# Optimization experiments

Measured on AMD Instinct MI355X. Metric: run time of the kernel, lower is better.

Reference implementation:

```python
import jax, jax.numpy as jnp
import numpy as np

WORD_VOCAB, WORD_DIM = 50257, 512
CHAR_VOCAB, CHAR_DIM = 262, 128
OUT_DIM = 1024
B, SW, SC = 32, 256, 16
EMB_DIM = WORD_DIM + CHAR_DIM


def setup_inputs() -> dict:
    key = jax.random.key(0)
    ks = jax.random.split(key, 12)
    word_inputs = jax.random.randint(ks[0], (B, SW), 0, WORD_VOCAB)
    char_ids = jax.random.randint(ks[1], (B, SW, SC), 0, CHAR_VOCAB)
    char_lengths = jax.random.randint(ks[2], (B, SW), 1, SC + 1)  # at least 1 char
    word_table = jax.random.normal(ks[3], (WORD_VOCAB, WORD_DIM), jnp.float32) * 0.02
    char_table = jax.random.normal(ks[4], (CHAR_VOCAB, CHAR_DIM), jnp.float32) * 0.02
    # RecursiveCell: gate = Linear(2d -> 3d), project = Linear(2d -> d)
    Wg = jax.random.normal(ks[5], (3 * CHAR_DIM, 2 * CHAR_DIM), jnp.float32) * (1.0 / np.sqrt(2 * CHAR_DIM))
    bg = jnp.zeros((3 * CHAR_DIM,), jnp.float32)
    Wp = jax.random.normal(ks[6], (CHAR_DIM, 2 * CHAR_DIM), jnp.float32) * (1.0 / np.sqrt(2 * CHAR_DIM))
    bp = jnp.zeros((CHAR_DIM,), jnp.float32)
    # final projection Linear(emb_dim -> output_dim)
    W_out = jax.random.normal(ks[7], (OUT_DIM, EMB_DIM), jnp.float32) * (1.0 / np.sqrt(EMB_DIM))
    b_out = jnp.zeros((OUT_DIM,), jnp.float32)
    return {"word_inputs": word_inputs, "char_ids": char_ids, "char_lengths": char_lengths,
            "word_table": word_table, "char_table": char_table,
            "Wg": Wg, "bg": bg, "Wp": Wp, "bp": bp, "W_out": W_out, "b_out": b_out}


def reference(word_inputs, char_ids, char_lengths, word_table, char_table, Wg, bg, Wp, bp, W_out, b_out):
    b, sw = word_inputs.shape
    sc = char_ids.shape[-1]
    d = char_table.shape[-1]
    n = b * sw

    word_emb = word_table[word_inputs]                      # [B, SW, WORD_DIM]

    ids = char_ids.reshape(n, sc)
    lens = char_lengths.reshape(n, 1)
    layer0 = char_table[ids]                                # [N, SC, d]
    pos = jnp.arange(sc)

    def step(layer, length):
        # vectorized RecursiveCell over all adjacent pairs i in [0, SC-2]
        left = layer[:, :-1, :]                             # [N, SC-1, d]
        right = layer[:, 1:, :]                             # [N, SC-1, d]
        flat = jnp.concatenate([left, right], axis=-1)      # [N, SC-1, 2d]
        z = flat @ Wp.T + bp                                # [N, SC-1, d]
        g = jax.nn.softmax((flat @ Wg.T + bg).reshape(n, sc - 1, 3, d), axis=2)
        ret = g[:, :, 0] * left + g[:, :, 1] * right + g[:, :, 2] * z
        new_layer = jnp.pad(ret, ((0, 0), (0, 1), (0, 0)))  # positions >= SC-1 stay zero
        # masked_scatter_: update position i iff i < len - length
        mask = (pos[None, :] < (lens - length))[..., None]  # [N, SC, 1]
        return jnp.where(mask, new_layer, layer), None

    layer, _ = jax.lax.scan(step, layer0, jnp.arange(1, sc))
    char_repr = layer[:, 0, :].reshape(b, sw, d)            # [B, SW, d]

    token_embedding = jnp.concatenate([word_emb, char_repr], axis=-1)
    return token_embedding @ W_out.T + b_out                # [B, SW, OUT_DIM]
```

## Files before the change

### kernel.cpp

```cpp
#include <hip/hip_runtime.h>
#include <hip/hip_bf16.h>

#define NTOK 8192
#define SCC  16
#define CD   128
#define WD   512
#define OD   1024
#define ED   640
#define TW   4
#define SP   132
#define ST   (SCC * SP)

typedef __attribute__((ext_vector_type(8))) short short8;
typedef __attribute__((ext_vector_type(4))) float f32x4;

__device__ __forceinline__ unsigned short f2bf(float f) {
    union { float f; unsigned u; } v; v.f = f;
    unsigned r = v.u + 0x7FFF + ((v.u >> 16) & 1);
    return (unsigned short)(r >> 16);
}

__global__ void sort_zero(int* s) { if (threadIdx.x < 48) s[threadIdx.x] = 0; }

__global__ void sort_hist(const int* __restrict__ lengths, int* __restrict__ s) {
    const int i = blockIdx.x * 256 + threadIdx.x;
    if (i < NTOK) atomicAdd(&s[lengths[i] - 1], 1);
}

__global__ void sort_prefix(int* s) {
    if (threadIdx.x == 0) {
        int acc = 0;
        for (int b = 15; b >= 0; --b) { s[16 + b] = acc; acc += s[b]; }
    }
}

__global__ __launch_bounds__(256) void sort_scatter_det(
    const int* __restrict__ lengths, int* __restrict__ s)
{
    __shared__ int wsum[4];
    __shared__ int running;
    const int b   = blockIdx.x;
    const int tid = threadIdx.x;
    if (tid == 0) running = s[16 + b];
    __syncthreads();
    for (int c0 = 0; c0 < NTOK; c0 += 256) {
        const int i = c0 + tid;
        const bool f = (lengths[i] - 1 == b);
        const unsigned long long m = __ballot(f);
        const int wv = tid >> 6;
        if ((tid & 63) == 0) wsum[wv] = __popcll(m);
        __syncthreads();
        int excl = 0;
#pragma unroll
        for (int k = 0; k < 4; ++k) if (k < wv) excl += wsum[k];
        const int lanerank = __popcll(m & ((1ull << (tid & 63)) - 1ull));
        if (f) s[48 + running + excl + lanerank] = i;
        const int tot = wsum[0] + wsum[1] + wsum[2] + wsum[3];
        __syncthreads();
        if (tid == 0) running += tot;
        __syncthreads();
    }
}

__global__ __launch_bounds__(256) void pack_weights(
    const float* __restrict__ Wg, const float* __restrict__ Wp,
    uint4* __restrict__ packed)
{
    const int gid  = blockIdx.x * 256 + threadIdx.x;
    const int lane = gid & 63;
    const int kf   = (gid >> 6) & 7;
    const int c    = (gid >> 9) & 3;
    const int w    = (gid >> 11) & 7;
    const int n    = c * 128 + w * 16 + (lane & 15);
    const int k0   = kf * 32 + (lane >> 4) * 8;
    const float* src = (n < 384) ? (Wg + n * 256 + k0) : (Wp + (n - 384) * 256 + k0);
    uint4 o;
    o.x = f2bf(src[0]) | ((unsigned)f2bf(src[1]) << 16);
    o.y = f2bf(src[2]) | ((unsigned)f2bf(src[3]) << 16);
    o.z = f2bf(src[4]) | ((unsigned)f2bf(src[5]) << 16);
    o.w = f2bf(src[6]) | ((unsigned)f2bf(src[7]) << 16);
    packed[gid] = o;
}

__global__ __launch_bounds__(256) void pack_wout(
    const float* __restrict__ W_out, uint4* __restrict__ packed)
{
    const int gid  = blockIdx.x * 256 + threadIdx.x;
    const int lane = gid & 63;
    const int kf   = (gid >> 6) % 20;
    const int nb   = (gid >> 6) / 20;
    const int n    = nb * 16 + (lane & 15);
    const int k0   = kf * 32 + (lane >> 4) * 8;
    const float* src = W_out + (size_t)n * ED + k0;
    uint4 o;
    o.x = f2bf(src[0]) | ((unsigned)f2bf(src[1]) << 16);
    o.y = f2bf(src[2]) | ((unsigned)f2bf(src[3]) << 16);
    o.z = f2bf(src[4]) | ((unsigned)f2bf(src[5]) << 16);
    o.w = f2bf(src[6]) | ((unsigned)f2bf(src[7]) << 16);
    packed[gid] = o;
}

#define LOAD_B(DST, KF)                                                     \
    {                                                                       \
        const uint4* wp_ = Wpacked + (w * 32 + (KF)) * 64 + lane;           \
        union { uint4 u; short8 s; } cv0, cv1, cv2, cv3;                    \
        cv0.u = wp_[0];    DST[0] = cv0.s;                                  \
        cv1.u = wp_[512];  DST[1] = cv1.s;                                  \
        cv2.u = wp_[1024]; DST[2] = cv2.s;                                  \
        cv3.u = wp_[1536]; DST[3] = cv3.s;                                  \
    }

#define LOAD_B_LDS(DST, KFI)                                                \
    {                                                                       \
        const uint4* sp_ = SW + ((w * 3 + (KFI)) * 4) * 64 + lane;          \
        union { uint4 u; short8 s; } d0, d1, d2, d3;                        \
        d0.u = sp_[0];   DST[0] = d0.s;                                     \
        d1.u = sp_[64];  DST[1] = d1.s;                                     \
        d2.u = sp_[128]; DST[2] = d2.s;                                     \
        d3.u = sp_[192]; DST[3] = d3.s;                                     \
    }

#define MFMA_PHASE(BV, KF)                                                  \
    {                                                                       \
        _Pragma("unroll")                                                   \
        for (int m_ = 0; m_ < 4; ++m_) {                                    \
            if (m_ < mfrags) {                                              \
                const int r_ = m_ * 16 + col + (((KF) >= 4) ? 4 : 0);       \
                int ba_ = (r_ << 8) + (((KF) & 3) << 6) + (q << 4);         \
                ba_ ^= (r_ & 15) << 4;                                      \
                const short8 a_ = *reinterpret_cast<const short8*>(         \
                    reinterpret_cast<const char*>(X) + ba_);                \
                acc[m_][0] = __builtin_amdgcn_mfma_f32_16x16x32_bf16(a_, BV[0], acc[m_][0], 0, 0, 0); \
                acc[m_][1] = __builtin_amdgcn_mfma_f32_16x16x32_bf16(a_, BV[1], acc[m_][1], 0, 0, 0); \
                acc[m_][2] = __builtin_amdgcn_mfma_f32_16x16x32_bf16(a_, BV[2], acc[m_][2], 0, 0, 0); \
                acc[m_][3] = __builtin_amdgcn_mfma_f32_16x16x32_bf16(a_, BV[3], acc[m_][3], 0, 0, 0); \
            }                                                               \
        }                                                                   \
    }

__global__ __launch_bounds__(512, 2) void scan_mfma(
    const int*   __restrict__ char_ids,
    const int*   __restrict__ char_lengths,
    const float* __restrict__ char_table,
    const float* __restrict__ bg, const float* __restrict__ bp,
    const uint4* __restrict__ Wpacked,
    const int*   __restrict__ order,
    unsigned short* __restrict__ char_repr)
{
    __shared__ __align__(16) float S[TW * ST];
    __shared__ __align__(16) unsigned short X[68 * 128];
    __shared__ __align__(16) uint4 SW[8 * 3 * 4 * 64];
    __shared__ int toksh[TW];
    __shared__ int Lsh[TW];

    const int tid  = threadIdx.x;
    const int lane = tid & 63;
    const int w    = tid >> 6;
    const int col  = lane & 15;
    const int q    = lane >> 4;

    if (tid < TW) {
        const int tok = order[blockIdx.x * TW + tid];
        toksh[tid] = tok;
        Lsh[tid]   = char_lengths[tok];
    }

    const int dj = w * 16 + col;
    const float b02 = bg[dj] - bg[256 + dj];
    const float b12 = bg[128 + dj] - bg[256 + dj];
    const float bz  = bp[dj];

    short8 bpin0[4], bpin1[4];
    LOAD_B(bpin0, 0);
    LOAD_B(bpin1, 1);

#pragma unroll
    for (int kfi = 0; kfi < 3; ++kfi)
#pragma unroll
        for (int c = 0; c < 4; ++c)
            SW[((w * 3 + kfi) * 4 + c) * 64 + lane] =
                Wpacked[(w * 32 + c * 8 + (2 + kfi)) * 64 + lane];

    __syncthreads();

    for (int i = tid; i < TW * SCC * (CD / 4); i += 512) {
        const int t   = i >> 9;
        const int rem = i & 511;
        const int c   = rem >> 5;
        const int d4  = rem & 31;
        const int id  = char_ids[toksh[t] * SCC + c];
        const float4 v = reinterpret_cast<const float4*>(char_table + id * CD)[d4];
        *reinterpret_cast<float4*>(S + t * ST + c * SP + d4 * 4) = v;
    }

    int L[TW];
#pragma unroll
    for (int t = 0; t < TW; ++t) L[t] = Lsh[t];
    const int maxL = max(max(L[0], L[1]), max(L[2], L[3]));

    __syncthreads();

    for (int i = tid; i < 68 * 64; i += 512) {
        const int r  = i >> 6;
        const int ku = i & 63;
        unsigned u = 0u;
        if (r < 60) {
            const int p = r >> 2, t = r & 3;
            const float2 v = *reinterpret_cast<const float2*>(S + t * ST + p * SP + 2 * ku);
            u = f2bf(v.x) | ((unsigned)f2bf(v.y) << 16);
        }
        int ba = (r << 8) + (ku << 2);
        ba ^= (r & 15) << 4;
        *reinterpret_cast<unsigned*>(reinterpret_cast<char*>(X) + ba) = u;
    }
    __syncthreads();

    for (int len = 1; len < maxL; ++len) {
        const int Amax   = maxL - len;
        const int mfrags = (4 * Amax + 15) >> 4;

        f32x4 acc[4][4];
#pragma unroll
        for (int m = 0; m < 4; ++m)
#pragma unroll
            for (int c = 0; c < 4; ++c) acc[m][c] = (f32x4){0.f, 0.f, 0.f, 0.f};

        short8 bA[4], bB[4], bL[4];
        LOAD_B(bA, 5);
        LOAD_B(bB, 6);
        MFMA_PHASE(bpin0, 0);
        LOAD_B_LDS(bL, 0);
        MFMA_PHASE(bpin1, 1);
        MFMA_PHASE(bL, 2);
        LOAD_B_LDS(bL, 1);
        MFMA_PHASE(bL, 3);
        LOAD_B_LDS(bL, 2);
        MFMA_PHASE(bL, 4);
        MFMA_PHASE(bA, 5);
        LOAD_B(bA, 7);
        MFMA_PHASE(bB, 6);
        MFMA_PHASE(bA, 7);

#pragma unroll
        for (int m = 0; m < 4; ++m) {
            if (m < mfrags) {
                const int p = m * 4 + q;
#pragma unroll
                for (int i = 0; i < 4; ++i) {
                    const float a0  = acc[m][0][i];
                    const float a1  = acc[m][1][i];
                    const float a2v = acc[m][2][i];
                    const float z   = acc[m][3][i] + bz;
                    const float E0  = __expf(a0 - a2v + b02);
                    const float E1  = __expf(a1 - a2v + b12);
                    const float left  = S[i * ST + p * SP + dj];
                    const float right = S[i * ST + (p + 1) * SP + dj];
                    const float inv = __builtin_amdgcn_rcpf(E0 + E1 + 1.0f);
                    acc[m][0][i] = (E0 * left + E1 * right + z) * inv;
                }
            }
        }
        __syncthreads();

#pragma unroll
        for (int m = 0; m < 4; ++m) {
            if (m < mfrags) {
                const int p = m * 4 + q;
#pragma unroll
                for (int i = 0; i < 4; ++i) {
                    const float val = acc[m][0][i];
                    if (p < L[i] - len) S[i * ST + p * SP + dj] = val;
                    const unsigned short bv = f2bf(val);
                    const int rl = m * 16 + q * 4 + i;
                    int bl = (rl << 8) + (dj << 1);
                    bl ^= (rl & 15) << 4;
                    *reinterpret_cast<unsigned short*>(
                        reinterpret_cast<char*>(X) + bl) = bv;
                }
            }
        }
        __syncthreads();
    }

    for (int i = tid; i < TW * CD; i += 512) {
        const int t = i >> 7, d = i & 127;
        char_repr[toksh[t] * CD + d] = f2bf(S[t * ST + d]);
    }
}

__global__ __launch_bounds__(256) void out_mfma(
    const int*   __restrict__ word_inputs,
    const float* __restrict__ word_table,
    const unsigned short* __restrict__ char_repr,
    const uint4* __restrict__ pwout,
    const float* __restrict__ b_out,
    float*       __restrict__ out)
{
    __shared__ __align__(16) unsigned short E[16 * ED];

    const int tg   = blockIdx.x * 16;
    const int tid  = threadIdx.x;
    const int lane = tid & 63;
    const int w    = tid >> 6;
    const int col  = lane & 15;
    const int q    = lane >> 4;

    for (int i = tid; i < 16 * 256; i += 256) {
        const int rt = i >> 8, kp = i & 255;
        const float2 v = *reinterpret_cast<const float2*>(
            word_table + (size_t)word_inputs[tg + rt] * WD + 2 * kp);
        const unsigned u = f2bf(v.x) | ((unsigned)f2bf(v.y) << 16);
        int baddr = rt * 1280 + kp * 4;
        baddr ^= (rt & 7) << 4;
        *reinterpret_cast<unsigned*>(reinterpret_cast<char*>(E) + baddr) = u;
    }
    for (int i = tid; i < 16 * 64; i += 256) {
        const int rt = i >> 6, kp = i & 63;
        const unsigned u = *reinterpret_cast<const unsigned*>(
            char_repr + (tg + rt) * CD + 2 * kp);
        int baddr = rt * 1280 + 1024 + kp * 4;
        baddr ^= (rt & 7) << 4;
        *reinterpret_cast<unsigned*>(reinterpret_cast<char*>(E) + baddr) = u;
    }
    __syncthreads();

    f32x4 acc[16];
#pragma unroll
    for (int nf = 0; nf < 16; ++nf) acc[nf] = (f32x4){0.f, 0.f, 0.f, 0.f};

#pragma unroll 4
    for (int kf = 0; kf < 20; ++kf) {
        int ba = col * 1280 + kf * 64 + q * 16;
        ba ^= (col & 7) << 4;
        const short8 a = *reinterpret_cast<const short8*>(
            reinterpret_cast<const char*>(E) + ba);
#pragma unroll
        for (int nf = 0; nf < 16; ++nf) {
            const int nb = w * 16 + nf;
            union { uint4 u; short8 s; } cv;
            cv.u = pwout[(nb * 20 + kf) * 64 + lane];
            acc[nf] = __builtin_amdgcn_mfma_f32_16x16x32_bf16(a, cv.s, acc[nf], 0, 0, 0);
        }
    }

#pragma unroll
    for (int nf = 0; nf < 16; ++nf) {
        const int j = (w * 16 + nf) * 16 + col;
        const float bias = b_out[j];
#pragma unroll
        for (int i = 0; i < 4; ++i) {
            out[(size_t)(tg + q * 4 + i) * OD + j] = acc[nf][i] + bias;
        }
    }
}


extern "C" void kernel_launch(void* const* d_in, const int* in_sizes, int n_in,
                              void* d_out, int out_size, void* d_ws, size_t ws_size,
                              hipStream_t stream)
{
    const int*   word_inputs  = (const int*)  d_in[0];
    const int*   char_ids     = (const int*)  d_in[1];
    const int*   char_lengths = (const int*)  d_in[2];
    const float* word_table   = (const float*)d_in[3];
    const float* char_table   = (const float*)d_in[4];
    const float* Wg           = (const float*)d_in[5];
    const float* bg           = (const float*)d_in[6];
    const float* Wp           = (const float*)d_in[7];
    const float* bp           = (const float*)d_in[8];
    const float* W_out        = (const float*)d_in[9];
    const float* b_out        = (const float*)d_in[10];

    float* out = (float*)d_out;
    char* ws = (char*)d_ws;
    unsigned short* char_repr = (unsigned short*)ws;
    uint4* Wpacked = (uint4*)(ws + 2 * 1024 * 1024);
    int*   sortbuf = (int*)(ws + 2 * 1024 * 1024 + 256 * 1024);
    const int* order = sortbuf + 48;
    uint4* pwout = (uint4*)(ws + 2 * 1024 * 1024 + 256 * 1024 + 64 * 1024);

    pack_weights<<<64, 256, 0, stream>>>(Wg, Wp, Wpacked);
    pack_wout<<<320, 256, 0, stream>>>(W_out, pwout);
    sort_zero<<<1, 64, 0, stream>>>(sortbuf);
    sort_hist<<<NTOK / 256, 256, 0, stream>>>(char_lengths, sortbuf);
    sort_prefix<<<1, 64, 0, stream>>>(sortbuf);
    sort_scatter_det<<<16, 256, 0, stream>>>(char_lengths, sortbuf);

    scan_mfma<<<NTOK / TW, 512, 0, stream>>>(char_ids, char_lengths, char_table,
                                             bg, bp, Wpacked, order, char_repr);
    out_mfma<<<NTOK / 16, 256, 0, stream>>>(word_inputs, word_table, char_repr,
                                            pwout, b_out, out);
}
```

Before: 270.9 us.

## Keep scan state in registers with shuffles; retile output GEMM to 32 tokens

```diff
diff --git a/kernel.cpp b/kernel.cpp
--- a/kernel.cpp
+++ b/kernel.cpp
@@ -8,8 +8,6 @@
 #define OD   1024
 #define ED   640
 #define TW   4
-#define SP   132
-#define ST   (SCC * SP)
 
 typedef __attribute__((ext_vector_type(8))) short short8;
 typedef __attribute__((ext_vector_type(4))) float f32x4;
@@ -147,7 +145,6 @@
     const int*   __restrict__ order,
     unsigned short* __restrict__ char_repr)
 {
-    __shared__ __align__(16) float S[TW * ST];
     __shared__ __align__(16) unsigned short X[68 * 128];
     __shared__ __align__(16) uint4 SW[8 * 3 * 4 * 64];
     __shared__ int toksh[TW];
@@ -183,35 +180,37 @@
 
     __syncthreads();
 
-    for (int i = tid; i < TW * SCC * (CD / 4); i += 512) {
-        const int t   = i >> 9;
-        const int rem = i & 511;
-        const int c   = rem >> 5;
-        const int d4  = rem & 31;
-        const int id  = char_ids[toksh[t] * SCC + c];
-        const float4 v = reinterpret_cast<const float4*>(char_table + id * CD)[d4];
-        *reinterpret_cast<float4*>(S + t * ST + c * SP + d4 * 4) = v;
-    }
-
     int L[TW];
 #pragma unroll
-    for (int t = 0; t < TW; ++t) L[t] = Lsh[t];
+    for (int i = 0; i < TW; ++i) L[i] = Lsh[i];
     const int maxL = max(max(L[0], L[1]), max(L[2], L[3]));
 
-    __syncthreads();
-
-    for (int i = tid; i < 68 * 64; i += 512) {
-        const int r  = i >> 6;
-        const int ku = i & 63;
-        unsigned u = 0u;
-        if (r < 60) {
-            const int p = r >> 2, t = r & 3;
-            const float2 v = *reinterpret_cast<const float2*>(S + t * ST + p * SP + 2 * ku);
-            u = f2bf(v.x) | ((unsigned)f2bf(v.y) << 16);
-        }
+    float stv[4][4];
+#pragma unroll
+    for (int m = 0; m < 4; ++m) {
+        const int p = m * 4 + q;
+#pragma unroll
+        for (int i = 0; i < 4; ++i) {
+            const int id = char_ids[toksh[i] * SCC + p];
+            stv[m][i] = char_table[id * CD + dj];
+        }
+    }
+
+#pragma unroll
+    for (int m = 0; m < 4; ++m)
+#pragma unroll
+        for (int i = 0; i < 4; ++i) {
+            const int rl = m * 16 + q * 4 + i;
+            int bl = (rl << 8) + (dj << 1);
+            bl ^= (rl & 15) << 4;
+            *reinterpret_cast<unsigned short*>(reinterpret_cast<char*>(X) + bl) =
+                f2bf(stv[m][i]);
+        }
+    for (int i2 = tid; i2 < 4 * 64; i2 += 512) {
+        const int r = 64 + (i2 >> 6), ku = i2 & 63;
         int ba = (r << 8) + (ku << 2);
         ba ^= (r & 15) << 4;
-        *reinterpret_cast<unsigned*>(reinterpret_cast<char*>(X) + ba) = u;
+        *reinterpret_cast<unsigned*>(reinterpret_cast<char*>(X) + ba) = 0u;
     }
     __syncthreads();
 
@@ -241,6 +240,15 @@
         MFMA_PHASE(bB, 6);
         MFMA_PHASE(bA, 7);
 
+        float shifted[5][4];
+#pragma unroll
+        for (int m = 0; m < 4; ++m)
+#pragma unroll
+            for (int i = 0; i < 4; ++i)
+                shifted[m][i] = __shfl(stv[m][i], (lane + 16) & 63);
+#pragma unroll
+        for (int i = 0; i < 4; ++i) shifted[4][i] = 0.f;
+
 #pragma unroll
         for (int m = 0; m < 4; ++m) {
             if (m < mfrags) {
@@ -253,10 +261,11 @@
                     const float z   = acc[m][3][i] + bz;
                     const float E0  = __expf(a0 - a2v + b02);
                     const float E1  = __expf(a1 - a2v + b12);
-                    const float left  = S[i * ST + p * SP + dj];
-                    const float right = S[i * ST + (p + 1) * SP + dj];
+                    const float left  = stv[m][i];
+                    const float right = (q < 3) ? shifted[m][i] : shifted[m + 1][i];
                     const float inv = __builtin_amdgcn_rcpf(E0 + E1 + 1.0f);
-                    acc[m][0][i] = (E0 * left + E1 * right + z) * inv;
+                    const float nv  = (E0 * left + E1 * right + z) * inv;
+                    stv[m][i] = (p < L[i] - len) ? nv : stv[m][i];
                 }
             }
         }
@@ -265,30 +274,29 @@
 #pragma unroll
         for (int m = 0; m < 4; ++m) {
             if (m < mfrags) {
-                const int p = m * 4 + q;
 #pragma unroll
                 for (int i = 0; i < 4; ++i) {
-                    const float val = acc[m][0][i];
-                    if (p < L[i] - len) S[i * ST + p * SP + dj] = val;
-                    const unsigned short bv = f2bf(val);
                     const int rl = m * 16 + q * 4 + i;
                     int bl = (rl << 8) + (dj << 1);
                     bl ^= (rl & 15) << 4;
                     *reinterpret_cast<unsigned short*>(
-                        reinterpret_cast<char*>(X) + bl) = bv;
+                        reinterpret_cast<char*>(X) + bl) = f2bf(stv[m][i]);
                 }
             }
         }
         __syncthreads();
     }
 
-    for (int i = tid; i < TW * CD; i += 512) {
-        const int t = i >> 7, d = i & 127;
-        char_repr[toksh[t] * CD + d] = f2bf(S[t * ST + d]);
-    }
-}
-
-__global__ __launch_bounds__(256) void out_mfma(
+    if (q == 0) {
+#pragma unroll
+        for (int i = 0; i < 4; ++i)
+            char_repr[toksh[i] * CD + dj] = f2bf(stv[0][i]);
+    }
+}
+
+#define TPB2 32
+
+__global__ __launch_bounds__(512) void out_mfma(
     const int*   __restrict__ word_inputs,
     const float* __restrict__ word_table,
     const unsigned short* __restrict__ char_repr,
@@ -296,16 +304,16 @@
     const float* __restrict__ b_out,
     float*       __restrict__ out)
 {
-    __shared__ __align__(16) unsigned short E[16 * ED];
-
-    const int tg   = blockIdx.x * 16;
+    __shared__ __align__(16) unsigned short E[TPB2 * ED];
+
+    const int tg   = blockIdx.x * TPB2;
     const int tid  = threadIdx.x;
     const int lane = tid & 63;
     const int w    = tid >> 6;
     const int col  = lane & 15;
     const int q    = lane >> 4;
 
-    for (int i = tid; i < 16 * 256; i += 256) {
+    for (int i = tid; i < TPB2 * 256; i += 512) {
         const int rt = i >> 8, kp = i & 255;
         const float2 v = *reinterpret_cast<const float2*>(
             word_table + (size_t)word_inputs[tg + rt] * WD + 2 * kp);
@@ -314,7 +322,7 @@
         baddr ^= (rt & 7) << 4;
         *reinterpret_cast<unsigned*>(reinterpret_cast<char*>(E) + baddr) = u;
     }
-    for (int i = tid; i < 16 * 64; i += 256) {
+    for (int i = tid; i < TPB2 * 64; i += 512) {
         const int rt = i >> 6, kp = i & 63;
         const unsigned u = *reinterpret_cast<const unsigned*>(
             char_repr + (tg + rt) * CD + 2 * kp);
@@ -324,33 +332,43 @@
     }
     __syncthreads();
 
-    f32x4 acc[16];
-#pragma unroll
-    for (int nf = 0; nf < 16; ++nf) acc[nf] = (f32x4){0.f, 0.f, 0.f, 0.f};
+    f32x4 acc[2][8];
+#pragma unroll
+    for (int mm = 0; mm < 2; ++mm)
+#pragma unroll
+        for (int nf = 0; nf < 8; ++nf) acc[mm][nf] = (f32x4){0.f, 0.f, 0.f, 0.f};
 
 #pragma unroll 4
     for (int kf = 0; kf < 20; ++kf) {
-        int ba = col * 1280 + kf * 64 + q * 16;
-        ba ^= (col & 7) << 4;
-        const short8 a = *reinterpret_cast<const short8*>(
-            reinterpret_cast<const char*>(E) + ba);
-#pragma unroll
-        for (int nf = 0; nf < 16; ++nf) {
-            const int nb = w * 16 + nf;
+        short8 a[2];
+#pragma unroll
+        for (int mm = 0; mm < 2; ++mm) {
+            const int row = mm * 16 + col;
+            int ba = row * 1280 + kf * 64 + q * 16;
+            ba ^= (row & 7) << 4;
+            a[mm] = *reinterpret_cast<const short8*>(
+                reinterpret_cast<const char*>(E) + ba);
+        }
+#pragma unroll
+        for (int nf = 0; nf < 8; ++nf) {
+            const int nb = w * 8 + nf;
             union { uint4 u; short8 s; } cv;
             cv.u = pwout[(nb * 20 + kf) * 64 + lane];
-            acc[nf] = __builtin_amdgcn_mfma_f32_16x16x32_bf16(a, cv.s, acc[nf], 0, 0, 0);
-        }
-    }
-
-#pragma unroll
-    for (int nf = 0; nf < 16; ++nf) {
-        const int j = (w * 16 + nf) * 16 + col;
+            acc[0][nf] = __builtin_amdgcn_mfma_f32_16x16x32_bf16(a[0], cv.s, acc[0][nf], 0, 0, 0);
+            acc[1][nf] = __builtin_amdgcn_mfma_f32_16x16x32_bf16(a[1], cv.s, acc[1][nf], 0, 0, 0);
+        }
+    }
+
+#pragma unroll
+    for (int nf = 0; nf < 8; ++nf) {
+        const int j = (w * 8 + nf) * 16 + col;
         const float bias = b_out[j];
 #pragma unroll
-        for (int i = 0; i < 4; ++i) {
-            out[(size_t)(tg + q * 4 + i) * OD + j] = acc[nf][i] + bias;
-        }
+        for (int mm = 0; mm < 2; ++mm)
+#pragma unroll
+            for (int i = 0; i < 4; ++i) {
+                out[(size_t)(tg + mm * 16 + q * 4 + i) * OD + j] = acc[mm][nf][i] + bias;
+            }
     }
 }
 
@@ -388,6 +406,6 @@
 
     scan_mfma<<<NTOK / TW, 512, 0, stream>>>(char_ids, char_lengths, char_table,
                                              bg, bp, Wpacked, order, char_repr);
-    out_mfma<<<NTOK / 16, 256, 0, stream>>>(word_inputs, word_table, char_repr,
-                                            pwout, b_out, out);
-}
+    out_mfma<<<NTOK / TPB2, 512, 0, stream>>>(word_inputs, word_table, char_repr,
+                                              pwout, b_out, out);
+}
```

After: 267.8 us. About the same (-1.1%).
